# Performance work log

Measured on AMD Instinct MI355X. Metric: run time of the kernel, lower is better.

## Reference

```python
import jax, jax.numpy as jnp
import numpy as np


def rotate_half(x):
    # interleaved rotate: (x0,x1,x2,x3,...) -> (-x1,x0,-x3,x2,...)
    x1 = x[..., 0::2]
    x2 = x[..., 1::2]
    return jnp.stack((-x2, x1), axis=-1).reshape(x.shape)


def setup_inputs() -> dict:
    key = jax.random.key(0)
    B, T, C, H = 8, 2048, 2048, 128
    ks = jax.random.split(key, 4)
    x = jax.random.normal(ks[0], (B, T, C), dtype=jnp.float32)
    wq = jax.random.normal(ks[1], (C, H), dtype=jnp.float32) * (C ** -0.5)
    wk = jax.random.normal(ks[2], (C, H), dtype=jnp.float32) * (C ** -0.5)
    wv = jax.random.normal(ks[3], (C, H), dtype=jnp.float32) * (C ** -0.5)
    # standard RoPE tables, interleaved pairs share a frequency
    inv_freq = 1.0 / (10000.0 ** (np.arange(0, H, 2, dtype=np.float32) / H))  # [H/2]
    ang = np.arange(T, dtype=np.float32)[:, None] * inv_freq[None, :]          # [T, H/2]
    ang = np.repeat(ang, 2, axis=-1)                                           # [T, H]
    rope_cos = jnp.asarray(np.cos(ang), dtype=jnp.float32)
    rope_sin = jnp.asarray(np.sin(ang), dtype=jnp.float32)
    return {"x": x, "wq": wq, "wk": wk, "wv": wv,
            "rope_cos": rope_cos, "rope_sin": rope_sin}


def reference(x, wq, wk, wv, rope_cos, rope_sin):
    B, T, C = x.shape
    H = wq.shape[1]
    q = x @ wq  # [B,T,H]
    k = x @ wk
    cos = rope_cos[:T][None]  # [1,T,H]
    sin = rope_sin[:T][None]
    q = q * cos + rotate_half(q) * sin
    k = k * cos + rotate_half(k) * sin
    wei = jnp.einsum('bth,bsh->bts', q, k) / (H ** 0.5)  # [B,T,T]
    causal = jnp.tril(jnp.ones((T, T), dtype=bool))
    wei = jnp.where(causal[None], wei, -jnp.inf)
    wei = jax.nn.softmax(wei, axis=-1)
    v = x @ wv  # [B,T,H]
    out = jnp.einsum('bts,bsh->bth', wei, v)
    return out
```

## Files before the change

kernel.cpp:

```cpp
#include <hip/hip_runtime.h>
#include <hip/hip_bf16.h>

typedef __attribute__((ext_vector_type(8))) short bf16x8;
typedef __attribute__((ext_vector_type(8))) unsigned short u16x8;
typedef __attribute__((ext_vector_type(4))) unsigned short u16x4;
typedef __attribute__((ext_vector_type(4))) float f32x4;

__device__ __forceinline__ unsigned short f2bf(float f) {
    __hip_bfloat16 h = __float2bfloat16(f);
    return *reinterpret_cast<unsigned short*>(&h);
}

__device__ __forceinline__ void cp16(void* lds, const void* g) {
    __builtin_amdgcn_global_load_lds(
        (const __attribute__((address_space(1))) unsigned int*)g,
        (__attribute__((address_space(3))) unsigned int*)lds, 16, 0, 0);
}

__global__ __launch_bounds__(256) void pack_w(
    const float* __restrict__ wq, const float* __restrict__ wk,
    const float* __restrict__ wv, unsigned short* __restrict__ wt)
{
    int idx = blockIdx.x * 256 + threadIdx.x;
    int n   = idx & 127;
    int k   = (idx >> 7) & 2047;
    int sel = idx >> 18;
    const float* w = (sel == 0) ? wq : (sel == 1) ? wk : wv;
    wt[(size_t)(sel * 128 + n) * 2048 + k] = f2bf(w[k * 128 + n]);
}

__global__ __launch_bounds__(256) void qkv_gemm(
    const float* __restrict__ x, const unsigned short* __restrict__ wt,
    const float* __restrict__ rc, const float* __restrict__ rs,
    unsigned short* __restrict__ Qb, unsigned short* __restrict__ Kb,
    unsigned short* __restrict__ VT)
{
    __shared__ __align__(16) float          As[3][128 * 32];
    __shared__ __align__(16) unsigned short Bs[3][128 * 32];

    const int bid   = blockIdx.x;
    const int slot  = bid & 7;
    const int idx   = bid >> 3;
    const int mtile = slot + 8 * (idx / 3);
    const int ntile = idx % 3;

    const int tid  = threadIdx.x;
    const int lane = tid & 63;
    const int wid  = tid >> 6;
    const int wm   = wid >> 1, wn = wid & 1;
    const int grp  = lane >> 4, cl = lane & 15;

    const float*          xb = x  + (size_t)(mtile * 128) * 2048;
    const unsigned short* wb = wt + (size_t)(ntile * 128) * 2048;

    auto stage = [&](int buf, int ks) {
        #pragma unroll
        for (int it = 0; it < 4; ++it) {
            int i   = tid + it * 256;
            int row = i >> 3;
            int cs  = (i & 7) ^ (row & 7);
            cp16((char*)&As[buf][0] + i * 16,
                 xb + (size_t)row * 2048 + ks * 32 + cs * 4);
        }
        #pragma unroll
        for (int it = 0; it < 2; ++it) {
            int i  = tid + it * 256;
            int n  = i >> 2;
            int cs = (i & 3) ^ ((n >> 1) & 3);
            cp16((char*)&Bs[buf][0] + i * 16,
                 (const char*)(wb + (size_t)n * 2048 + ks * 32) + cs * 16);
        }
    };

    const f32x4 fz = {0.f, 0.f, 0.f, 0.f};
    f32x4 acc[4][4];
    #pragma unroll
    for (int mf = 0; mf < 4; ++mf)
        #pragma unroll
        for (int nf = 0; nf < 4; ++nf) acc[mf][nf] = fz;

    stage(0, 0);
    stage(1, 1);
    asm volatile("s_waitcnt vmcnt(6)" ::: "memory");
    __builtin_amdgcn_s_barrier();

    for (int ks = 0; ks < 64; ++ks) {
        const int cur = ks % 3;
        if (ks + 2 < 64) stage((ks + 2) % 3, ks + 2);

        bf16x8 a[4], b[4];
        #pragma unroll
        for (int mf = 0; mf < 4; ++mf) {
            int row = wm * 64 + mf * 16 + cl;
            int c0  = (2 * grp)     ^ (row & 7);
            int c1  = (2 * grp + 1) ^ (row & 7);
            const float* ab = &As[cur][row * 32];
            f32x4 lo = *reinterpret_cast<const f32x4*>(ab + c0 * 4);
            f32x4 hi = *reinterpret_cast<const f32x4*>(ab + c1 * 4);
            bf16x8 av;
            av[0] = (short)f2bf(lo[0]); av[1] = (short)f2bf(lo[1]);
            av[2] = (short)f2bf(lo[2]); av[3] = (short)f2bf(lo[3]);
            av[4] = (short)f2bf(hi[0]); av[5] = (short)f2bf(hi[1]);
            av[6] = (short)f2bf(hi[2]); av[7] = (short)f2bf(hi[3]);
            a[mf] = av;
        }
        #pragma unroll
        for (int nf = 0; nf < 4; ++nf) {
            int n  = wn * 64 + nf * 16 + cl;
            int sl = grp ^ ((n >> 1) & 3);
            b[nf] = *reinterpret_cast<const bf16x8*>(&Bs[cur][n * 32 + sl * 8]);
        }
        #pragma unroll
        for (int mf = 0; mf < 4; ++mf)
            #pragma unroll
            for (int nf = 0; nf < 4; ++nf)
                acc[mf][nf] = __builtin_amdgcn_mfma_f32_16x16x32_bf16(
                    a[mf], b[nf], acc[mf][nf], 0, 0, 0);

        if (ks < 63) {
            if (ks + 2 < 64) {
                asm volatile("s_waitcnt vmcnt(6)" ::: "memory");
            } else {
                asm volatile("s_waitcnt vmcnt(0)" ::: "memory");
            }
            asm volatile("s_waitcnt lgkmcnt(0)" ::: "memory");
            __builtin_amdgcn_s_barrier();
        }
    }

    if (ntile == 0) {
        #pragma unroll
        for (int mf = 0; mf < 4; ++mf) {
            int mrow = mtile * 128 + wm * 64 + mf * 16 + grp * 4;
            #pragma unroll
            for (int nf = 0; nf < 4; ++nf) {
                int h = wn * 64 + nf * 16 + cl;
                #pragma unroll
                for (int r = 0; r < 4; ++r) {
                    int   m   = mrow + r;
                    int   t   = m & 2047;
                    float val = acc[mf][nf][r];
                    float pr  = __shfl_xor(val, 1, 64);
                    float cs  = rc[t * 128 + h];
                    float sn  = rs[t * 128 + h];
                    float res = (h & 1) ? fmaf(val, cs, pr * sn)
                                        : fmaf(val, cs, -pr * sn);
                    Qb[(size_t)m * 128 + h] = f2bf(res);
                }
            }
        }
    } else if (ntile == 1) {
        #pragma unroll
        for (int mf = 0; mf < 4; ++mf) {
            int mrow = mtile * 128 + wm * 64 + mf * 16 + grp * 4;
            #pragma unroll
            for (int nf = 0; nf < 4; ++nf) {
                int h = wn * 64 + nf * 16 + cl;
                #pragma unroll
                for (int r = 0; r < 4; ++r) {
                    int   m   = mrow + r;
                    int   t   = m & 2047;
                    float val = acc[mf][nf][r];
                    float pr  = __shfl_xor(val, 1, 64);
                    float cs  = rc[t * 128 + h];
                    float sn  = rs[t * 128 + h];
                    float res = (h & 1) ? fmaf(val, cs, pr * sn)
                                        : fmaf(val, cs, -pr * sn);
                    int bo = h * 2;
                    int bs = (bo & 128) | ((bo & 127) ^ ((m & 7) << 4));
                    *(unsigned short*)((char*)Kb + (size_t)m * 256 + bs) = f2bf(res);
                }
            }
        }
    } else {
        #pragma unroll
        for (int mf = 0; mf < 4; ++mf) {
            int mrow = mtile * 128 + wm * 64 + mf * 16 + grp * 4;
            int bb   = mrow >> 11;
            int t0   = mrow & 2047;
            #pragma unroll
            for (int nf = 0; nf < 4; ++nf) {
                int h = wn * 64 + nf * 16 + cl;
                u16x4 pk;
                #pragma unroll
                for (int r = 0; r < 4; ++r) pk[r] = f2bf(acc[mf][nf][r]);
                int bo = (t0 * 2) & 127;
                int bs = ((t0 * 2) & ~127) | (bo ^ ((h & 7) << 4));
                *reinterpret_cast<u16x4*>(
                    (char*)VT + (size_t)(bb * 128 + h) * 4096 + bs) = pk;
            }
        }
    }
}

__global__ __launch_bounds__(256, 2) void flash_attn(
    const unsigned short* __restrict__ Qb, const unsigned short* __restrict__ Kb,
    const unsigned short* __restrict__ VT, float* __restrict__ Op,
    float2* __restrict__ ML, float* __restrict__ out, int nchunk)
{
    __shared__ __align__(16) unsigned short Ks[2][64 * 128];
    __shared__ __align__(16) unsigned short Vs[2][128 * 64];
    __shared__ __align__(16) unsigned short Ps[4][16 * 72];

    const int g      = blockIdx.x;
    const int per_mt = 8 * nchunk;
    const int mtd    = g / per_mt;
    const int mt     = 31 - mtd;
    const int rem    = g - mtd * per_mt;
    const int c      = rem >> 3;
    const int b      = rem & 7;

    const int tid  = threadIdx.x;
    const int lane = tid & 63;
    const int w    = tid >> 6;
    const int grp  = lane >> 4, cl = lane & 15;

    const int NT   = mt + 1;
    const int T0   = (NT + 1) >> 1;
    const int tbeg = (nchunk == 2 && c == 1) ? T0 : 0;
    const int tend = (nchunk == 2 && c == 0) ? T0 : NT;

    const int   q0    = mt * 64 + w * 16;
    const float scale = 0.08838834764831845f;

    bf16x8 aq[4];
    {
        const unsigned short* qp = Qb + (size_t)(b * 2048 + q0 + cl) * 128 + grp * 8;
        #pragma unroll
        for (int kc = 0; kc < 4; ++kc)
            aq[kc] = *reinterpret_cast<const bf16x8*>(qp + kc * 32);
    }

    const f32x4 fz = {0.f, 0.f, 0.f, 0.f};
    f32x4 o[8];
    #pragma unroll
    for (int nf = 0; nf < 8; ++nf) o[nf] = fz;
    float mrun[4], lrun[4];
    #pragma unroll
    for (int r = 0; r < 4; ++r) { mrun[r] = -INFINITY; lrun[r] = 0.f; }

    const char* kgb = (const char*)(Kb + (size_t)b * 2048 * 128);
    const char* vgb = (const char*)(VT + (size_t)b * 128 * 2048);

    auto stage = [&](int d, int t) {
        const char* ks = kgb + (size_t)t * 64 * 256;
        char* kd = (char*)&Ks[d][0];
        #pragma unroll
        for (int i = 0; i < 4; ++i) {
            int off = w * 4096 + i * 1024 + lane * 16;
            cp16(kd + off, ks + off);
        }
        const char* vsb = vgb + (size_t)t * 128;
        char* vd = (char*)&Vs[d][0];
        #pragma unroll
        for (int i = 0; i < 4; ++i) {
            int off = w * 4096 + i * 1024 + lane * 16;
            cp16(vd + off, vsb + (size_t)(off >> 7) * 4096 + (off & 127));
        }
    };

    if (tbeg < tend) stage(0, tbeg);
    __syncthreads();

    int cur = 0;
    for (int t = tbeg; t < tend; ++t) {
        if (t + 1 < tend) stage(cur ^ 1, t + 1);

        const char* kb   = (const char*)&Ks[cur][0];
        const char* vb   = (const char*)&Vs[cur][0];
        const bool  diag = (t == mt);
        const int   jmax = diag ? (w + 1) : 4;

        float p[4][4];
        float mx[4];
        #pragma unroll
        for (int r = 0; r < 4; ++r) mx[r] = -INFINITY;

        #pragma unroll
        for (int j = 0; j < 4; ++j) {
            #pragma unroll
            for (int r = 0; r < 4; ++r) p[j][r] = 0.f;
            if (j < jmax) {
                int   row = j * 16 + cl;
                f32x4 s   = fz;
                #pragma unroll
                for (int kc = 0; kc < 4; ++kc) {
                    int bo = kc * 64 + grp * 16;
                    int bs = (bo & 128) | ((bo & 127) ^ ((row & 7) << 4));
                    bf16x8 kf = *reinterpret_cast<const bf16x8*>(kb + row * 256 + bs);
                    s = __builtin_amdgcn_mfma_f32_16x16x32_bf16(aq[kc], kf, s, 0, 0, 0);
                }
                #pragma unroll
                for (int r = 0; r < 4; ++r) {
                    float a = s[r] * scale;
                    if (diag && j == w && cl > grp * 4 + r) a = -INFINITY;
                    p[j][r] = a;
                    mx[r]   = fmaxf(mx[r], a);
                }
            }
        }
        #pragma unroll
        for (int d = 1; d < 16; d <<= 1)
            #pragma unroll
            for (int r = 0; r < 4; ++r)
                mx[r] = fmaxf(mx[r], __shfl_xor(mx[r], d, 64));

        float alpha[4], psum[4];
        #pragma unroll
        for (int r = 0; r < 4; ++r) {
            float mn = fmaxf(mrun[r], mx[r]);
            alpha[r] = __expf(mrun[r] - mn);
            mrun[r]  = mn;
            psum[r]  = 0.f;
        }
        #pragma unroll
        for (int j = 0; j < 4; ++j)
            if (j < jmax)
                #pragma unroll
                for (int r = 0; r < 4; ++r) {
                    p[j][r] = __expf(p[j][r] - mrun[r]);
                    psum[r] += p[j][r];
                }
        #pragma unroll
        for (int d = 1; d < 16; d <<= 1)
            #pragma unroll
            for (int r = 0; r < 4; ++r)
                psum[r] += __shfl_xor(psum[r], d, 64);
        #pragma unroll
        for (int r = 0; r < 4; ++r)
            lrun[r] = lrun[r] * alpha[r] + psum[r];
        #pragma unroll
        for (int nf = 0; nf < 8; ++nf)
            #pragma unroll
            for (int r = 0; r < 4; ++r) o[nf][r] *= alpha[r];

        char* pwb = (char*)&Ps[w][0];
        #pragma unroll
        for (int j = 0; j < 4; ++j)
            #pragma unroll
            for (int r = 0; r < 4; ++r) {
                int prow = grp * 4 + r;
                int bytec = ((j * 16 + cl) * 2) ^ ((prow & 7) << 4);
                *reinterpret_cast<unsigned short*>(pwb + prow * 144 + bytec) =
                    f2bf(p[j][r]);
            }

        const char* pb = (const char*)&Ps[w][0];
        #pragma unroll
        for (int half = 0; half < 2; ++half) {
            int pbo = half * 64 + grp * 16;
            bf16x8 pa = *reinterpret_cast<const bf16x8*>(
                pb + cl * 144 + (pbo ^ ((cl & 7) << 4)));
            #pragma unroll
            for (int nf = 0; nf < 8; ++nf) {
                int h  = nf * 16 + cl;
                int bs = (half * 64 + grp * 16) ^ ((h & 7) << 4);
                bf16x8 vf = *reinterpret_cast<const bf16x8*>(vb + h * 128 + bs);
                o[nf] = __builtin_amdgcn_mfma_f32_16x16x32_bf16(pa, vf, o[nf], 0, 0, 0);
            }
        }
        __syncthreads();
        cur ^= 1;
    }

    if (nchunk == 2) {
        #pragma unroll
        for (int nf = 0; nf < 8; ++nf)
            #pragma unroll
            for (int r = 0; r < 4; ++r) {
                size_t rowg = (size_t)c * 16384 + b * 2048 + q0 + grp * 4 + r;
                Op[rowg * 128 + nf * 16 + cl] = o[nf][r];
            }
        if (cl == 0)
            #pragma unroll
            for (int r = 0; r < 4; ++r)
                ML[(size_t)c * 16384 + b * 2048 + q0 + grp * 4 + r] =
                    make_float2(mrun[r], lrun[r]);
    } else {
        float inv[4];
        #pragma unroll
        for (int r = 0; r < 4; ++r) inv[r] = 1.0f / lrun[r];
        #pragma unroll
        for (int nf = 0; nf < 8; ++nf)
            #pragma unroll
            for (int r = 0; r < 4; ++r)
                out[(size_t)(b * 2048 + q0 + grp * 4 + r) * 128 + nf * 16 + cl] =
                    o[nf][r] * inv[r];
    }
}

__global__ __launch_bounds__(256) void merge2(
    const float* __restrict__ Op, const float2* __restrict__ ML,
    float* __restrict__ out)
{
    int idx = blockIdx.x * 256 + threadIdx.x;
    int row = idx >> 5, hq = idx & 31;
    float2 ml0 = ML[row];
    float2 ml1 = ML[16384 + row];
    float  m  = fmaxf(ml0.x, ml1.x);
    float  e0 = __expf(ml0.x - m);
    float  e1 = __expf(ml1.x - m);
    float  inv = 1.0f / (ml0.y * e0 + ml1.y * e1);
    f32x4 o0 = *reinterpret_cast<const f32x4*>(Op + (size_t)row * 128 + hq * 4);
    f32x4 o1 = *reinterpret_cast<const f32x4*>(Op + ((size_t)16384 + row) * 128 + hq * 4);
    f32x4 res;
    #pragma unroll
    for (int i = 0; i < 4; ++i) res[i] = (o0[i] * e0 + o1[i] * e1) * inv;
    *reinterpret_cast<f32x4*>(out + (size_t)row * 128 + hq * 4) = res;
}

extern "C" void kernel_launch(void* const* d_in, const int* in_sizes, int n_in,
                              void* d_out, int out_size, void* d_ws, size_t ws_size,
                              hipStream_t stream)
{
    const float* x  = (const float*)d_in[0];
    const float* wq = (const float*)d_in[1];
    const float* wk = (const float*)d_in[2];
    const float* wv = (const float*)d_in[3];
    const float* rc = (const float*)d_in[4];
    const float* rs = (const float*)d_in[5];
    float* out = (float*)d_out;

    char* ws = (char*)d_ws;
    const size_t MB = 1u << 20;
    unsigned short* wt = (unsigned short*)(ws);
    unsigned short* Qb = (unsigned short*)(ws + 2 * MB);
    unsigned short* Kb = (unsigned short*)(ws + 6 * MB);
    unsigned short* VT = (unsigned short*)(ws + 10 * MB);
    float*          Op = (float*)        (ws + 14 * MB);
    float2*         ML = (float2*)       (ws + 30 * MB);

    const int nchunk = (ws_size >= (size_t)31 * MB) ? 2 : 1;

    pack_w  <<<3072, 256, 0, stream>>>(wq, wk, wv, wt);
    qkv_gemm<<<384,  256, 0, stream>>>(x, wt, rc, rs, Qb, Kb, VT);
    flash_attn<<<32 * 8 * nchunk, 256, 0, stream>>>(Qb, Kb, VT, Op, ML, out, nchunk);
    if (nchunk == 2)
        merge2<<<2048, 256, 0, stream>>>(Op, ML, out);
}
```

Baseline: 128.9 us.

## Retile QKV GEMM to 64x384 blocks so each x tile is loaded once

```diff
diff --git a/kernel.cpp b/kernel.cpp
--- a/kernel.cpp
+++ b/kernel.cpp
@@ -29,42 +29,36 @@
     wt[(size_t)(sel * 128 + n) * 2048 + k] = f2bf(w[k * 128 + n]);
 }
 
-__global__ __launch_bounds__(256) void qkv_gemm(
+__global__ __launch_bounds__(512) void qkv_gemm(
     const float* __restrict__ x, const unsigned short* __restrict__ wt,
     const float* __restrict__ rc, const float* __restrict__ rs,
     unsigned short* __restrict__ Qb, unsigned short* __restrict__ Kb,
     unsigned short* __restrict__ VT)
 {
-    __shared__ __align__(16) float          As[3][128 * 32];
-    __shared__ __align__(16) unsigned short Bs[3][128 * 32];
-
-    const int bid   = blockIdx.x;
-    const int slot  = bid & 7;
-    const int idx   = bid >> 3;
-    const int mtile = slot + 8 * (idx / 3);
-    const int ntile = idx % 3;
-
+    __shared__ __align__(16) float          As[3][64 * 32];
+    __shared__ __align__(16) unsigned short Bs[3][384 * 32];
+
+    const int mtile = blockIdx.x;
     const int tid  = threadIdx.x;
     const int lane = tid & 63;
-    const int wid  = tid >> 6;
-    const int wm   = wid >> 1, wn = wid & 1;
+    const int w    = tid >> 6;
+    const int wm   = w >> 2, wn = w & 3;
     const int grp  = lane >> 4, cl = lane & 15;
 
-    const float*          xb = x  + (size_t)(mtile * 128) * 2048;
-    const unsigned short* wb = wt + (size_t)(ntile * 128) * 2048;
+    const float*          xb = x + (size_t)(mtile * 64) * 2048;
+    const unsigned short* wb = wt;
 
     auto stage = [&](int buf, int ks) {
-        #pragma unroll
-        for (int it = 0; it < 4; ++it) {
-            int i   = tid + it * 256;
+        {
+            int i   = tid;
             int row = i >> 3;
             int cs  = (i & 7) ^ (row & 7);
             cp16((char*)&As[buf][0] + i * 16,
                  xb + (size_t)row * 2048 + ks * 32 + cs * 4);
         }
         #pragma unroll
-        for (int it = 0; it < 2; ++it) {
-            int i  = tid + it * 256;
+        for (int it = 0; it < 3; ++it) {
+            int i  = tid + it * 512;
             int n  = i >> 2;
             int cs = (i & 3) ^ ((n >> 1) & 3);
             cp16((char*)&Bs[buf][0] + i * 16,
@@ -73,25 +67,25 @@
     };
 
     const f32x4 fz = {0.f, 0.f, 0.f, 0.f};
-    f32x4 acc[4][4];
+    f32x4 acc[2][6];
     #pragma unroll
-    for (int mf = 0; mf < 4; ++mf)
-        #pragma unroll
-        for (int nf = 0; nf < 4; ++nf) acc[mf][nf] = fz;
+    for (int mf = 0; mf < 2; ++mf)
+        #pragma unroll
+        for (int nf = 0; nf < 6; ++nf) acc[mf][nf] = fz;
 
     stage(0, 0);
     stage(1, 1);
-    asm volatile("s_waitcnt vmcnt(6)" ::: "memory");
+    asm volatile("s_waitcnt vmcnt(4)" ::: "memory");
     __builtin_amdgcn_s_barrier();
 
     for (int ks = 0; ks < 64; ++ks) {
         const int cur = ks % 3;
         if (ks + 2 < 64) stage((ks + 2) % 3, ks + 2);
 
-        bf16x8 a[4], b[4];
-        #pragma unroll
-        for (int mf = 0; mf < 4; ++mf) {
-            int row = wm * 64 + mf * 16 + cl;
+        bf16x8 a[2], b[6];
+        #pragma unroll
+        for (int mf = 0; mf < 2; ++mf) {
+            int row = wm * 32 + mf * 16 + cl;
             int c0  = (2 * grp)     ^ (row & 7);
             int c1  = (2 * grp + 1) ^ (row & 7);
             const float* ab = &As[cur][row * 32];
@@ -105,85 +99,61 @@
             a[mf] = av;
         }
         #pragma unroll
-        for (int nf = 0; nf < 4; ++nf) {
-            int n  = wn * 64 + nf * 16 + cl;
+        for (int nf = 0; nf < 6; ++nf) {
+            int n  = wn * 96 + nf * 16 + cl;
             int sl = grp ^ ((n >> 1) & 3);
             b[nf] = *reinterpret_cast<const bf16x8*>(&Bs[cur][n * 32 + sl * 8]);
         }
         #pragma unroll
-        for (int mf = 0; mf < 4; ++mf)
-            #pragma unroll
-            for (int nf = 0; nf < 4; ++nf)
+        for (int mf = 0; mf < 2; ++mf)
+            #pragma unroll
+            for (int nf = 0; nf < 6; ++nf)
                 acc[mf][nf] = __builtin_amdgcn_mfma_f32_16x16x32_bf16(
                     a[mf], b[nf], acc[mf][nf], 0, 0, 0);
 
         if (ks < 63) {
             if (ks + 2 < 64) {
-                asm volatile("s_waitcnt vmcnt(6)" ::: "memory");
+                asm volatile("s_waitcnt vmcnt(4)" ::: "memory");
             } else {
                 asm volatile("s_waitcnt vmcnt(0)" ::: "memory");
             }
-            asm volatile("s_waitcnt lgkmcnt(0)" ::: "memory");
             __builtin_amdgcn_s_barrier();
         }
     }
 
-    if (ntile == 0) {
-        #pragma unroll
-        for (int mf = 0; mf < 4; ++mf) {
-            int mrow = mtile * 128 + wm * 64 + mf * 16 + grp * 4;
-            #pragma unroll
-            for (int nf = 0; nf < 4; ++nf) {
-                int h = wn * 64 + nf * 16 + cl;
+    #pragma unroll
+    for (int mf = 0; mf < 2; ++mf) {
+        int mrow = mtile * 64 + wm * 32 + mf * 16 + grp * 4;
+        int bb   = mrow >> 11;
+        #pragma unroll
+        for (int nf = 0; nf < 6; ++nf) {
+            int nbase = wn * 96 + nf * 16;
+            int sel   = nbase >> 7;
+            int h     = (nbase & 127) + cl;
+            if (sel < 2) {
                 #pragma unroll
                 for (int r = 0; r < 4; ++r) {
                     int   m   = mrow + r;
-                    int   t   = m & 2047;
+                    int   tr  = m & 2047;
                     float val = acc[mf][nf][r];
                     float pr  = __shfl_xor(val, 1, 64);
-                    float cs  = rc[t * 128 + h];
-                    float sn  = rs[t * 128 + h];
+                    float cs  = rc[tr * 128 + h];
+                    float sn  = rs[tr * 128 + h];
                     float res = (h & 1) ? fmaf(val, cs, pr * sn)
                                         : fmaf(val, cs, -pr * sn);
-                    Qb[(size_t)m * 128 + h] = f2bf(res);
+                    if (sel == 0) {
+                        Qb[(size_t)m * 128 + h] = f2bf(res);
+                    } else {
+                        int bo = h * 2;
+                        int bs = (bo & 128) | ((bo & 127) ^ ((m & 7) << 4));
+                        *(unsigned short*)((char*)Kb + (size_t)m * 256 + bs) = f2bf(res);
+                    }
                 }
-            }
-        }
-    } else if (ntile == 1) {
-        #pragma unroll
-        for (int mf = 0; mf < 4; ++mf) {
-            int mrow = mtile * 128 + wm * 64 + mf * 16 + grp * 4;
-            #pragma unroll
-            for (int nf = 0; nf < 4; ++nf) {
-                int h = wn * 64 + nf * 16 + cl;
-                #pragma unroll
-                for (int r = 0; r < 4; ++r) {
-                    int   m   = mrow + r;
-                    int   t   = m & 2047;
-                    float val = acc[mf][nf][r];
-                    float pr  = __shfl_xor(val, 1, 64);
-                    float cs  = rc[t * 128 + h];
-                    float sn  = rs[t * 128 + h];
-                    float res = (h & 1) ? fmaf(val, cs, pr * sn)
-                                        : fmaf(val, cs, -pr * sn);
-                    int bo = h * 2;
-                    int bs = (bo & 128) | ((bo & 127) ^ ((m & 7) << 4));
-                    *(unsigned short*)((char*)Kb + (size_t)m * 256 + bs) = f2bf(res);
-                }
-            }
-        }
-    } else {
-        #pragma unroll
-        for (int mf = 0; mf < 4; ++mf) {
-            int mrow = mtile * 128 + wm * 64 + mf * 16 + grp * 4;
-            int bb   = mrow >> 11;
-            int t0   = mrow & 2047;
-            #pragma unroll
-            for (int nf = 0; nf < 4; ++nf) {
-                int h = wn * 64 + nf * 16 + cl;
+            } else {
                 u16x4 pk;
                 #pragma unroll
                 for (int r = 0; r < 4; ++r) pk[r] = f2bf(acc[mf][nf][r]);
+                int t0 = mrow & 2047;
                 int bo = (t0 * 2) & 127;
                 int bs = ((t0 * 2) & ~127) | (bo ^ ((h & 7) << 4));
                 *reinterpret_cast<u16x4*>(
@@ -433,7 +403,7 @@
     const int nchunk = (ws_size >= (size_t)31 * MB) ? 2 : 1;
 
     pack_w  <<<3072, 256, 0, stream>>>(wq, wk, wv, wt);
-    qkv_gemm<<<384,  256, 0, stream>>>(x, wt, rc, rs, Qb, Kb, VT);
+    qkv_gemm<<<256,  512, 0, stream>>>(x, wt, rc, rs, Qb, Kb, VT);
     flash_attn<<<32 * 8 * nchunk, 256, 0, stream>>>(Qb, Kb, VT, Op, ML, out, nchunk);
     if (nchunk == 2)
         merge2<<<2048, 256, 0, stream>>>(Op, ML, out);
```

New measurement: 131.9 us. 2.3% more time.
